# Performance work log

Measured on AMD Instinct MI355X. Metric: run time of the kernel, lower is better.

## Reference

```python
import jax, jax.numpy as jnp
import numpy as np

B, C, H, W = 1, 1, 1024, 1024
NP = 16                    # n_patches
S = NP * NP                # 256 tokens
D = 2048                   # hidden_d
NH = 16                    # heads
DH = D // NH               # 128
MLP = 4 * D
NB = 2                     # blocks
INPUT_D = C * (H // NP) * (W // NP)  # 4096
EPS = 1e-5


def positional_embeddings(s, d):
    # result[i,j] = sin(i/10000**(j/d)) if j even else cos(i/10000**((j-1)/d))
    i = jnp.arange(s, dtype=jnp.float32)[:, None]
    j = jnp.arange(d, dtype=jnp.float32)[None, :]
    even = (jnp.arange(d) % 2 == 0)[None, :]
    expo = jnp.where(even, j, j - 1.0) / d
    ang = i / (10000.0 ** expo)
    return jnp.where(even, jnp.sin(ang), jnp.cos(ang))


def layer_norm(x, g, b):
    m = x.mean(-1, keepdims=True)
    v = ((x - m) ** 2).mean(-1, keepdims=True)
    return (x - m) / jnp.sqrt(v + EPS) * g + b


def setup_inputs() -> dict:
    key = jax.random.key(0)
    ks = jax.random.split(key, 20)
    s = 0.02
    return {
        "images": jax.random.normal(ks[0], (B, C, H, W), jnp.float32),
        "memory": jax.random.normal(ks[1], (1, 8), jnp.float32),
        "wmap": jax.random.normal(ks[2], (INPUT_D, D), jnp.float32) * s,
        "bmap": jnp.zeros((D,), jnp.float32),
        "ln1_g": jnp.ones((NB, D), jnp.float32),
        "ln1_b": jnp.zeros((NB, D), jnp.float32),
        "qw": jax.random.normal(ks[3], (NB, NH, DH, DH), jnp.float32) * s,
        "qb": jnp.zeros((NB, NH, DH), jnp.float32),
        "kw": jax.random.normal(ks[4], (NB, NH, DH, DH), jnp.float32) * s,
        "kb": jnp.zeros((NB, NH, DH), jnp.float32),
        "vw": jax.random.normal(ks[5], (NB, NH, DH, DH), jnp.float32) * s,
        "vb": jnp.zeros((NB, NH, DH), jnp.float32),
        "ln2_g": jnp.ones((NB, D), jnp.float32),
        "ln2_b": jnp.zeros((NB, D), jnp.float32),
        "w1": jax.random.normal(ks[6], (NB, D, MLP), jnp.float32) * s,
        "b1": jnp.zeros((NB, MLP), jnp.float32),
        "w2": jax.random.normal(ks[7], (NB, MLP, D), jnp.float32) * s,
        "b2": jnp.zeros((NB, D), jnp.float32),
        "head_w": jax.random.normal(ks[8], (D, 1), jnp.float32) * s,
        "head_b": jnp.zeros((1,), jnp.float32),
    }


def reference(images, memory, wmap, bmap, ln1_g, ln1_b, qw, qb, kw, kb, vw, vb,
              ln2_g, ln2_b, w1, b1, w2, b2, head_w, head_b):
    # patchify: view(1, n_patches**2, num_h*num_v) -> (1, 256, 4096)
    patches = images.reshape(1, S, INPUT_D)
    tokens = patches @ wmap + bmap                      # (1, S, D)
    x = tokens + positional_embeddings(S, D)
    scale = DH ** 0.5
    for l in range(NB):
        h = layer_norm(x, ln1_g[l], ln1_b[l])
        h4 = h.reshape(B, S, NH, DH)
        q = jnp.einsum('bshd,hde->bshe', h4, qw[l]) + qb[l]
        k = jnp.einsum('bshd,hde->bshe', h4, kw[l]) + kb[l]
        v = jnp.einsum('bshd,hde->bshe', h4, vw[l]) + vb[l]
        att = jax.nn.softmax(jnp.einsum('bshe,bthe->bhst', q, k) / scale, axis=-1)
        attn_out = jnp.einsum('bhst,bthe->bshe', att, v).reshape(B, S, D)
        x = x + attn_out
        h2 = layer_norm(x, ln2_g[l], ln2_b[l])
        x = x + (jax.nn.gelu(h2 @ w1[l] + b1[l], approximate=False) @ w2[l] + b2[l])
    cls = x[:, 0]                                       # (1, D)
    out = jax.nn.sigmoid(cls @ head_w + head_b)         # (1, 1)
    return (out, memory)
```

## Files before the change

kernel.cpp:

```cpp
#include <hip/hip_runtime.h>
#include <math.h>

#define SQ   256
#define DD   2048
#define NHD  16
#define DHD  128
#define MLPD 8192
#define KIN  4096
#define INV_SQRT_DH 0.08838834764831845f

typedef __attribute__((ext_vector_type(8))) short bf16x8;
typedef __attribute__((ext_vector_type(4))) float f32x4;

__device__ __forceinline__ float gelu_f(float x) {
    return 0.5f * x * (1.0f + erff(x * 0.70710678118654752f));
}

__device__ __forceinline__ short f2bf(float f) {
    unsigned u = __float_as_uint(f);
    unsigned r = (u + 0x7fffu + ((u >> 16) & 1u)) >> 16;
    return (short)r;
}

__global__ __launch_bounds__(256) void gemm_splitk(const float* __restrict__ A,
                                                   const float* __restrict__ W,
                                                   float* __restrict__ C,
                                                   int N, int K, int KC) {
    __shared__ short As[64 * 64];
    __shared__ short Bs[64 * 64];
    const int tid = threadIdx.x;
    const int n0 = blockIdx.x * 64, m0 = blockIdx.y * 64;
    const int kstart = blockIdx.z * KC;
    const int wv = tid >> 6, ln = tid & 63;
    const int l15 = ln & 15, q = ln >> 4;

    f32x4 acc[4];
    #pragma unroll
    for (int j = 0; j < 4; j++) acc[j] = (f32x4){0.f, 0.f, 0.f, 0.f};

    const int am = tid >> 2, akb = (tid & 3) * 16, ac0 = (tid & 3) * 2;
    const int bn = tid & 63, bkb = (tid >> 6) * 16, bc0 = (tid >> 6) * 2;
    short* as0 = &As[am * 64 + ((ac0 ^ (am & 7)) * 8)];
    short* as1 = &As[am * 64 + (((ac0 + 1) ^ (am & 7)) * 8)];
    short* bs0 = &Bs[bn * 64 + ((bc0 ^ (bn & 7)) * 8)];
    short* bs1 = &Bs[bn * 64 + (((bc0 + 1) ^ (bn & 7)) * 8)];
    const int arow = 16 * wv + l15;
    const short* af0 = &As[arow * 64 + ((q ^ (arow & 7)) * 8)];
    const short* af1 = &As[arow * 64 + (((q + 4) ^ (arow & 7)) * 8)];

    for (int kc = kstart; kc < kstart + KC; kc += 64) {
        const float* ap = A + (size_t)(m0 + am) * K + kc + akb;
        float4 a0 = *(const float4*)ap;
        float4 a1 = *(const float4*)(ap + 4);
        float4 a2 = *(const float4*)(ap + 8);
        float4 a3 = *(const float4*)(ap + 12);
        const float* wp = W + (size_t)(kc + bkb) * N + n0 + bn;
        float wb[16];
        #pragma unroll
        for (int j = 0; j < 16; j++) wb[j] = wp[(size_t)j * N];

        __syncthreads();
        {
            short t[16] = {f2bf(a0.x), f2bf(a0.y), f2bf(a0.z), f2bf(a0.w),
                           f2bf(a1.x), f2bf(a1.y), f2bf(a1.z), f2bf(a1.w),
                           f2bf(a2.x), f2bf(a2.y), f2bf(a2.z), f2bf(a2.w),
                           f2bf(a3.x), f2bf(a3.y), f2bf(a3.z), f2bf(a3.w)};
            *(bf16x8*)as0 = *(bf16x8*)&t[0];
            *(bf16x8*)as1 = *(bf16x8*)&t[8];
            short u[16];
            #pragma unroll
            for (int j = 0; j < 16; j++) u[j] = f2bf(wb[j]);
            *(bf16x8*)bs0 = *(bf16x8*)&u[0];
            *(bf16x8*)bs1 = *(bf16x8*)&u[8];
        }
        __syncthreads();

        bf16x8 fa0 = *(const bf16x8*)af0;
        bf16x8 fa1 = *(const bf16x8*)af1;
        #pragma unroll
        for (int jt = 0; jt < 4; jt++) {
            const int brow = 16 * jt + l15;
            bf16x8 fb0 = *(const bf16x8*)&Bs[brow * 64 + ((q ^ (brow & 7)) * 8)];
            bf16x8 fb1 = *(const bf16x8*)&Bs[brow * 64 + (((q + 4) ^ (brow & 7)) * 8)];
            acc[jt] = __builtin_amdgcn_mfma_f32_16x16x32_bf16(fa0, fb0, acc[jt], 0, 0, 0);
            acc[jt] = __builtin_amdgcn_mfma_f32_16x16x32_bf16(fa1, fb1, acc[jt], 0, 0, 0);
        }
    }
    #pragma unroll
    for (int jt = 0; jt < 4; jt++) {
        const int n = n0 + 16 * jt + l15;
        #pragma unroll
        for (int i = 0; i < 4; i++) {
            const int m = m0 + 16 * wv + q * 4 + i;
            atomicAdd(&C[(size_t)m * N + n], acc[jt][i]);
        }
    }
}

__global__ __launch_bounds__(256) void epi_pos(float* __restrict__ x,
                                               const float* __restrict__ bmap) {
    const int idx = blockIdx.x * 256 + threadIdx.x;
    const int m = idx >> 11, n = idx & 2047;
    float val = x[idx] + bmap[n];
    float jf = (float)n;
    float expo = ((n & 1) ? (jf - 1.0f) : jf) * (1.0f / 2048.0f);
    float ang = (float)m * powf(10000.0f, -expo);
    x[idx] = val + ((n & 1) ? cosf(ang) : sinf(ang));
}

__global__ __launch_bounds__(256) void epi_gelu(float* __restrict__ y,
                                                const float* __restrict__ b1) {
    const int idx = blockIdx.x * 256 + threadIdx.x;
    y[idx] = gelu_f(y[idx] + b1[idx & 8191]);
}

__global__ __launch_bounds__(256) void epi_bias(float* __restrict__ x,
                                                const float* __restrict__ b2) {
    const int idx = blockIdx.x * 256 + threadIdx.x;
    x[idx] += b2[idx & 2047];
}

__global__ __launch_bounds__(256) void qkv_mfma(const float* __restrict__ h,
                                                const float* __restrict__ qw, const float* __restrict__ kw,
                                                const float* __restrict__ vw, const float* __restrict__ qb,
                                                const float* __restrict__ kb, const float* __restrict__ vb,
                                                float* __restrict__ q, float* __restrict__ k,
                                                float* __restrict__ v) {
    __shared__ short As[64 * 64];
    __shared__ short Bs[64 * 64];
    const int head = blockIdx.x, m0 = blockIdx.y * 64;
    const int type = blockIdx.z >> 1, n0 = (blockIdx.z & 1) * 64;
    const float* W; const float* B; float* O;
    if (type == 0)      { W = qw; B = qb; O = q; }
    else if (type == 1) { W = kw; B = kb; O = k; }
    else                { W = vw; B = vb; O = v; }
    W += (size_t)head * DHD * DHD;
    B += head * DHD;
    const int hoff = head * DHD;
    const int tid = threadIdx.x;
    const int wv = tid >> 6, ln = tid & 63;
    const int l15 = ln & 15, qq = ln >> 4;

    f32x4 acc[4];
    #pragma unroll
    for (int j = 0; j < 4; j++) acc[j] = (f32x4){0.f, 0.f, 0.f, 0.f};

    const int am = tid >> 2, akb = (tid & 3) * 16, ac0 = (tid & 3) * 2;
    const int bn = tid & 63, bkb = (tid >> 6) * 16, bc0 = (tid >> 6) * 2;
    short* as0 = &As[am * 64 + ((ac0 ^ (am & 7)) * 8)];
    short* as1 = &As[am * 64 + (((ac0 + 1) ^ (am & 7)) * 8)];
    short* bs0 = &Bs[bn * 64 + ((bc0 ^ (bn & 7)) * 8)];
    short* bs1 = &Bs[bn * 64 + (((bc0 + 1) ^ (bn & 7)) * 8)];
    const int arow = 16 * wv + l15;
    const short* af0 = &As[arow * 64 + ((qq ^ (arow & 7)) * 8)];
    const short* af1 = &As[arow * 64 + (((qq + 4) ^ (arow & 7)) * 8)];

    for (int kc = 0; kc < DHD; kc += 64) {
        const float* ap = h + (size_t)(m0 + am) * DD + hoff + kc + akb;
        float4 a0 = *(const float4*)ap;
        float4 a1 = *(const float4*)(ap + 4);
        float4 a2 = *(const float4*)(ap + 8);
        float4 a3 = *(const float4*)(ap + 12);
        const float* wp = W + (size_t)(kc + bkb) * DHD + n0 + bn;
        float wb[16];
        #pragma unroll
        for (int j = 0; j < 16; j++) wb[j] = wp[j * DHD];

        __syncthreads();
        {
            short t[16] = {f2bf(a0.x), f2bf(a0.y), f2bf(a0.z), f2bf(a0.w),
                           f2bf(a1.x), f2bf(a1.y), f2bf(a1.z), f2bf(a1.w),
                           f2bf(a2.x), f2bf(a2.y), f2bf(a2.z), f2bf(a2.w),
                           f2bf(a3.x), f2bf(a3.y), f2bf(a3.z), f2bf(a3.w)};
            *(bf16x8*)as0 = *(bf16x8*)&t[0];
            *(bf16x8*)as1 = *(bf16x8*)&t[8];
            short u[16];
            #pragma unroll
            for (int j = 0; j < 16; j++) u[j] = f2bf(wb[j]);
            *(bf16x8*)bs0 = *(bf16x8*)&u[0];
            *(bf16x8*)bs1 = *(bf16x8*)&u[8];
        }
        __syncthreads();

        bf16x8 fa0 = *(const bf16x8*)af0;
        bf16x8 fa1 = *(const bf16x8*)af1;
        #pragma unroll
        for (int jt = 0; jt < 4; jt++) {
            const int brow = 16 * jt + l15;
            bf16x8 fb0 = *(const bf16x8*)&Bs[brow * 64 + ((qq ^ (brow & 7)) * 8)];
            bf16x8 fb1 = *(const bf16x8*)&Bs[brow * 64 + (((qq + 4) ^ (brow & 7)) * 8)];
            acc[jt] = __builtin_amdgcn_mfma_f32_16x16x32_bf16(fa0, fb0, acc[jt], 0, 0, 0);
            acc[jt] = __builtin_amdgcn_mfma_f32_16x16x32_bf16(fa1, fb1, acc[jt], 0, 0, 0);
        }
    }
    #pragma unroll
    for (int jt = 0; jt < 4; jt++) {
        const int n = n0 + 16 * jt + l15;
        #pragma unroll
        for (int i = 0; i < 4; i++) {
            const int m = m0 + 16 * wv + qq * 4 + i;
            O[(size_t)m * DD + hoff + n] = acc[jt][i] + B[n];
        }
    }
}

__global__ __launch_bounds__(256) void attn_mfma(const float* __restrict__ q,
                                                 const float* __restrict__ k,
                                                 const float* __restrict__ v,
                                                 float* __restrict__ x) {
    __shared__ short P[64 * 272];
    __shared__ short ST[9216];
    const int head = blockIdx.y, r0 = blockIdx.x * 64;
    const int hoff = head * DHD;
    const int tid = threadIdx.x;
    const int wv = tid >> 6, ln = tid & 63;
    const int l15 = ln & 15, qd = ln >> 4;

    bf16x8 af[4];
    {
        const float* qp = q + (size_t)(r0 + 16 * wv + l15) * DD + hoff + qd * 8;
        #pragma unroll
        for (int s = 0; s < 4; s++) {
            float4 f0 = *(const float4*)(qp + s * 32);
            float4 f1 = *(const float4*)(qp + s * 32 + 4);
            short t[8] = {f2bf(f0.x), f2bf(f0.y), f2bf(f0.z), f2bf(f0.w),
                          f2bf(f1.x), f2bf(f1.y), f2bf(f1.z), f2bf(f1.w)};
            af[s] = *(bf16x8*)t;
        }
    }

    f32x4 sacc[16];
    #pragma unroll
    for (int i = 0; i < 16; i++) sacc[i] = (f32x4){0.f, 0.f, 0.f, 0.f};

    const int skey = tid >> 2, scol = (tid & 3) * 32;
    for (int kq = 0; kq < 4; kq++) {
        const float* kp = k + (size_t)(kq * 64 + skey) * DD + hoff + scol;
        float4 f[8];
        #pragma unroll
        for (int a = 0; a < 8; a++) f[a] = *(const float4*)(kp + a * 4);
        if (kq) __syncthreads();
        #pragma unroll
        for (int a = 0; a < 4; a++) {
            short t[8] = {f2bf(f[2*a].x), f2bf(f[2*a].y), f2bf(f[2*a].z), f2bf(f[2*a].w),
                          f2bf(f[2*a+1].x), f2bf(f[2*a+1].y), f2bf(f[2*a+1].z), f2bf(f[2*a+1].w)};
            *(bf16x8*)&ST[skey * 136 + scol + a * 8] = *(bf16x8*)t;
        }
        __syncthreads();
        #pragma unroll
        for (int nl = 0; nl < 4; nl++) {
            #pragma unroll
            for (int s = 0; s < 4; s++) {
                bf16x8 bfr = *(const bf16x8*)&ST[(nl * 16 + l15) * 136 + s * 32 + qd * 8];
                sacc[kq * 4 + nl] = __builtin_amdgcn_mfma_f32_16x16x32_bf16(af[s], bfr, sacc[kq * 4 + nl], 0, 0, 0);
            }
        }
    }

    float inv_s[4];
    #pragma unroll
    for (int i = 0; i < 4; i++) {
        float m = -1e30f;
        #pragma unroll
        for (int nt = 0; nt < 16; nt++) m = fmaxf(m, sacc[nt][i]);
        m = fmaxf(m, __shfl_xor(m, 1));
        m = fmaxf(m, __shfl_xor(m, 2));
        m = fmaxf(m, __shfl_xor(m, 4));
        m = fmaxf(m, __shfl_xor(m, 8));
        float sum = 0.f;
        #pragma unroll
        for (int nt = 0; nt < 16; nt++) {
            float e = __expf((sacc[nt][i] - m) * INV_SQRT_DH);
            sacc[nt][i] = e;
            sum += e;
        }
        sum += __shfl_xor(sum, 1);
        sum += __shfl_xor(sum, 2);
        sum += __shfl_xor(sum, 4);
        sum += __shfl_xor(sum, 8);
        inv_s[i] = 1.0f / sum;
    }
    #pragma unroll
    for (int nt = 0; nt < 16; nt++) {
        const int col = nt * 16 + l15;
        const int chunk = col >> 3, c7 = col & 7;
        #pragma unroll
        for (int i = 0; i < 4; i++) {
            const int row = 16 * wv + 4 * qd + i;
            P[row * 272 + ((chunk ^ (row & 7)) * 8) + c7] = f2bf(sacc[nt][i] * inv_s[i]);
        }
    }
    __syncthreads();

    f32x4 oacc[8];
    #pragma unroll
    for (int e = 0; e < 8; e++) oacc[e] = (f32x4){0.f, 0.f, 0.f, 0.f};

    const int ve = tid & 127, vks = (tid >> 7) * 32;
    for (int kq = 0; kq < 4; kq++) {
        float vv[32];
        #pragma unroll
        for (int j = 0; j < 32; j++)
            vv[j] = v[(size_t)(kq * 64 + vks + j) * DD + hoff + ve];
        if (kq) __syncthreads();
        #pragma unroll
        for (int c = 0; c < 4; c++) {
            short t[8];
            #pragma unroll
            for (int b = 0; b < 8; b++) t[b] = f2bf(vv[c * 8 + b]);
            const int ch = (vks >> 3) + c;
            *(bf16x8*)&ST[ve * 72 + ((ch ^ (ve & 7)) * 8)] = *(bf16x8*)t;
        }
        __syncthreads();
        #pragma unroll
        for (int s = 0; s < 2; s++) {
            const int row = 16 * wv + l15;
            const int pc = kq * 8 + s * 4 + qd;
            bf16x8 pa = *(const bf16x8*)&P[row * 272 + ((pc ^ (row & 7)) * 8)];
            #pragma unroll
            for (int et = 0; et < 8; et++) {
                const int er = et * 16 + l15;
                const int vc = s * 4 + qd;
                bf16x8 vb = *(const bf16x8*)&ST[er * 72 + ((vc ^ (er & 7)) * 8)];
                oacc[et] = __builtin_amdgcn_mfma_f32_16x16x32_bf16(pa, vb, oacc[et], 0, 0, 0);
            }
        }
    }
    #pragma unroll
    for (int et = 0; et < 8; et++) {
        const int e = et * 16 + l15;
        #pragma unroll
        for (int i = 0; i < 4; i++) {
            const int row = r0 + 16 * wv + 4 * qd + i;
            x[(size_t)row * DD + hoff + e] += oacc[et][i];
        }
    }
}

__global__ __launch_bounds__(256) void ln_kernel(const float* __restrict__ xin,
                                                 const float* __restrict__ g,
                                                 const float* __restrict__ b,
                                                 float* __restrict__ out,
                                                 float* __restrict__ zbuf, int zn) {
    __shared__ float red[8];
    const int tid = threadIdx.x;
    for (int i = tid; i < zn; i += 256) zbuf[i] = 0.0f;
    const int row = blockIdx.x;
    const float* xr = xin + row * DD;
    float vals[8];
    float s = 0.0f;
    #pragma unroll
    for (int i = 0; i < 8; i++) { vals[i] = xr[tid + i * 256]; s += vals[i]; }
    #pragma unroll
    for (int o = 32; o > 0; o >>= 1) s += __shfl_down(s, o);
    if ((tid & 63) == 0) red[tid >> 6] = s;
    __syncthreads();
    if (tid == 0) red[4] = (red[0] + red[1] + red[2] + red[3]) * (1.0f / 2048.0f);
    __syncthreads();
    const float mean = red[4];
    float vs = 0.0f;
    #pragma unroll
    for (int i = 0; i < 8; i++) { float d = vals[i] - mean; vs += d * d; }
    #pragma unroll
    for (int o = 32; o > 0; o >>= 1) vs += __shfl_down(vs, o);
    if ((tid & 63) == 0) red[tid >> 6] = vs;
    __syncthreads();
    if (tid == 0) red[5] = rsqrtf((red[0] + red[1] + red[2] + red[3]) * (1.0f / 2048.0f) + 1e-5f);
    __syncthreads();
    const float inv = red[5];
    #pragma unroll
    for (int i = 0; i < 8; i++) {
        int c = tid + i * 256;
        out[row * DD + c] = (vals[i] - mean) * inv * g[c] + b[c];
    }
}

__global__ __launch_bounds__(256) void attn0_kernel(const float* __restrict__ q,
                                                    const float* __restrict__ k,
                                                    const float* __restrict__ v,
                                                    float* __restrict__ x) {
    __shared__ float q0[128];
    __shared__ float p[256];
    __shared__ float red[8];
    const int h = blockIdx.x, tid = threadIdx.x, hoff = h * DHD;
    if (tid < 128) q0[tid] = q[hoff + tid];
    __syncthreads();
    const float* kr = k + tid * DD + hoff;
    float s = 0.0f;
    #pragma unroll 8
    for (int d = 0; d < 128; d++) s += q0[d] * kr[d];
    s *= INV_SQRT_DH;
    float m = s;
    #pragma unroll
    for (int o = 32; o > 0; o >>= 1) m = fmaxf(m, __shfl_down(m, o));
    if ((tid & 63) == 0) red[tid >> 6] = m;
    __syncthreads();
    if (tid == 0) red[4] = fmaxf(fmaxf(red[0], red[1]), fmaxf(red[2], red[3]));
    __syncthreads();
    const float mx = red[4];
    float e = __expf(s - mx);
    p[tid] = e;
    float t = e;
    #pragma unroll
    for (int o = 32; o > 0; o >>= 1) t += __shfl_down(t, o);
    if ((tid & 63) == 0) red[tid >> 6] = t;
    __syncthreads();
    if (tid == 0) red[5] = red[0] + red[1] + red[2] + red[3];
    __syncthreads();
    const float inv = 1.0f / red[5];
    if (tid < 128) {
        float acc = 0.0f;
        #pragma unroll 8
        for (int j = 0; j < 256; j++) acc += p[j] * v[j * DD + hoff + tid];
        x[hoff + tid] += acc * inv;
    }
}

__global__ __launch_bounds__(256) void gemv1_kernel(const float* __restrict__ h2,
                                                    const float* __restrict__ w1,
                                                    float* __restrict__ y) {
    const int n = blockIdx.x * 256 + threadIdx.x;
    const int k0 = blockIdx.y * 64;
    float s = 0.0f;
    #pragma unroll 8
    for (int k = 0; k < 64; k++) s += h2[k0 + k] * w1[(size_t)(k0 + k) * MLPD + n];
    atomicAdd(&y[n], s);
}

__global__ __launch_bounds__(256) void gelu_bias_kernel(float* __restrict__ y,
                                                        const float* __restrict__ b1) {
    const int n = blockIdx.x * 256 + threadIdx.x;
    y[n] = gelu_f(y[n] + b1[n]);
}

__global__ __launch_bounds__(256) void gemv2_kernel(const float* __restrict__ y1,
                                                    const float* __restrict__ w2,
                                                    float* __restrict__ x) {
    const int m = blockIdx.x * 256 + threadIdx.x;
    const int k0 = blockIdx.y * 256;
    float s = 0.0f;
    #pragma unroll 8
    for (int k = 0; k < 256; k++) s += y1[k0 + k] * w2[(size_t)(k0 + k) * DD + m];
    atomicAdd(&x[m], s);
}

__global__ __launch_bounds__(256) void head_kernel(const float* __restrict__ x,
                                                   const float* __restrict__ b2l,
                                                   const float* __restrict__ hw,
                                                   const float* __restrict__ hb,
                                                   const float* __restrict__ mem,
                                                   float* __restrict__ out) {
    __shared__ float red[8];
    const int tid = threadIdx.x;
    float s = 0.0f;
    for (int m = tid; m < 2048; m += 256) s += (x[m] + b2l[m]) * hw[m];
    #pragma unroll
    for (int o = 32; o > 0; o >>= 1) s += __shfl_down(s, o);
    if ((tid & 63) == 0) red[tid >> 6] = s;
    __syncthreads();
    if (tid == 0) {
        float t = red[0] + red[1] + red[2] + red[3];
        out[0] = 1.0f / (1.0f + __expf(-(t + hb[0])));
    }
    if (tid < 8) out[1 + tid] = mem[tid];
}

extern "C" void kernel_launch(void* const* d_in, const int* in_sizes, int n_in,
                              void* d_out, int out_size, void* d_ws, size_t ws_size,
                              hipStream_t stream) {
    const float* images = (const float*)d_in[0];
    const float* memory = (const float*)d_in[1];
    const float* wmap   = (const float*)d_in[2];
    const float* bmap   = (const float*)d_in[3];
    const float* ln1_g  = (const float*)d_in[4];
    const float* ln1_b  = (const float*)d_in[5];
    const float* qw     = (const float*)d_in[6];
    const float* qb     = (const float*)d_in[7];
    const float* kw     = (const float*)d_in[8];
    const float* kb     = (const float*)d_in[9];
    const float* vw     = (const float*)d_in[10];
    const float* vb     = (const float*)d_in[11];
    const float* ln2_g  = (const float*)d_in[12];
    const float* ln2_b  = (const float*)d_in[13];
    const float* w1     = (const float*)d_in[14];
    const float* b1     = (const float*)d_in[15];
    const float* w2     = (const float*)d_in[16];
    const float* b2     = (const float*)d_in[17];
    const float* head_w = (const float*)d_in[18];
    const float* head_b = (const float*)d_in[19];
    float* out = (float*)d_out;

    float* ws = (float*)d_ws;
    float* x     = ws;
    float* h     = x + SQ * DD;
    float* q     = h + SQ * DD;
    float* k     = q + SQ * DD;
    float* v     = k + SQ * DD;
    float* y1    = v + SQ * DD;
    float* y1row = y1 + SQ * MLPD;
    float* h2row = y1row + MLPD;

    hipMemsetAsync(x, 0, (size_t)SQ * DD * sizeof(float), stream);
    gemm_splitk<<<dim3(DD / 64, SQ / 64, 8), 256, 0, stream>>>(images, wmap, x, DD, KIN, 512);
    epi_pos<<<SQ * DD / 256, 256, 0, stream>>>(x, bmap);

    for (int l = 0; l < 2; l++) {
        const size_t wofs = (size_t)l * NHD * DHD * DHD;
        const size_t bofs = (size_t)l * NHD * DHD;
        ln_kernel<<<SQ, 256, 0, stream>>>(x, ln1_g + l * DD, ln1_b + l * DD, h, nullptr, 0);
        qkv_mfma<<<dim3(NHD, SQ / 64, 6), 256, 0, stream>>>(h, qw + wofs, kw + wofs, vw + wofs,
                                                            qb + bofs, kb + bofs, vb + bofs,
                                                            q, k, v);
        if (l == 0) {
            attn_mfma<<<dim3(SQ / 64, NHD), 256, 0, stream>>>(q, k, v, x);
            ln_kernel<<<SQ, 256, 0, stream>>>(x, ln2_g, ln2_b, h, nullptr, 0);
            hipMemsetAsync(y1, 0, (size_t)SQ * MLPD * sizeof(float), stream);
            gemm_splitk<<<dim3(MLPD / 64, SQ / 64, 2), 256, 0, stream>>>(h, w1, y1, MLPD, DD, 1024);
            epi_gelu<<<SQ * MLPD / 256, 256, 0, stream>>>(y1, b1);
            gemm_splitk<<<dim3(DD / 64, SQ / 64, 8), 256, 0, stream>>>(y1, w2, x, DD, MLPD, 1024);
            epi_bias<<<SQ * DD / 256, 256, 0, stream>>>(x, b2);
        } else {
            attn0_kernel<<<NHD, 256, 0, stream>>>(q, k, v, x);
            ln_kernel<<<1, 256, 0, stream>>>(x, ln2_g + DD, ln2_b + DD, h2row, y1row, MLPD);
            gemv1_kernel<<<dim3(MLPD / 256, 32), 256, 0, stream>>>(h2row, w1 + (size_t)DD * MLPD, y1row);
            gelu_bias_kernel<<<MLPD / 256, 256, 0, stream>>>(y1row, b1 + MLPD);
            gemv2_kernel<<<dim3(DD / 256, 32), 256, 0, stream>>>(y1row, w2 + (size_t)DD * MLPD, x);
            head_kernel<<<1, 256, 0, stream>>>(x, b2 + DD, head_w, head_b, memory, out);
        }
    }
}
```

Baseline: 508.3 us.

## Replace 64x64 split-K GEMM with double-buffered 128x128 tile GEMM

Swaps the 64x64-tile split-K GEMM for a 128x128-tile version with 512 threads, where each wave computes a 64x32 sub-tile. Shared-memory tiles are double-buffered and the next chunk's global loads are issued before the current chunk's MFMAs, so one sync per chunk replaces two. Larger tiles cut redundant global reads of A and W per FLOP, at the cost of a quarter as many blocks (fewer than CUs for the 2048-wide GEMMs) and more shared memory and registers per block.

```diff
diff --git a/kernel.cpp b/kernel.cpp
--- a/kernel.cpp
+++ b/kernel.cpp
@@ -22,77 +22,131 @@
     return (short)r;
 }
 
-__global__ __launch_bounds__(256) void gemm_splitk(const float* __restrict__ A,
-                                                   const float* __restrict__ W,
-                                                   float* __restrict__ C,
-                                                   int N, int K, int KC) {
-    __shared__ short As[64 * 64];
-    __shared__ short Bs[64 * 64];
+__global__ __launch_bounds__(512) void gemm128(const float* __restrict__ A,
+                                               const float* __restrict__ W,
+                                               float* __restrict__ C,
+                                               int N, int K, int KC) {
+    __shared__ short As[2][128 * 64];
+    __shared__ short Bs[2][128 * 64];
     const int tid = threadIdx.x;
-    const int n0 = blockIdx.x * 64, m0 = blockIdx.y * 64;
+    const int n0 = blockIdx.x * 128, m0 = blockIdx.y * 128;
     const int kstart = blockIdx.z * KC;
-    const int wv = tid >> 6, ln = tid & 63;
+    const int ln = tid & 63;
+    const int wv = tid >> 6;
     const int l15 = ln & 15, q = ln >> 4;
-
-    f32x4 acc[4];
-    #pragma unroll
-    for (int j = 0; j < 4; j++) acc[j] = (f32x4){0.f, 0.f, 0.f, 0.f};
-
-    const int am = tid >> 2, akb = (tid & 3) * 16, ac0 = (tid & 3) * 2;
-    const int bn = tid & 63, bkb = (tid >> 6) * 16, bc0 = (tid >> 6) * 2;
-    short* as0 = &As[am * 64 + ((ac0 ^ (am & 7)) * 8)];
-    short* as1 = &As[am * 64 + (((ac0 + 1) ^ (am & 7)) * 8)];
-    short* bs0 = &Bs[bn * 64 + ((bc0 ^ (bn & 7)) * 8)];
-    short* bs1 = &Bs[bn * 64 + (((bc0 + 1) ^ (bn & 7)) * 8)];
-    const int arow = 16 * wv + l15;
-    const short* af0 = &As[arow * 64 + ((q ^ (arow & 7)) * 8)];
-    const short* af1 = &As[arow * 64 + (((q + 4) ^ (arow & 7)) * 8)];
-
-    for (int kc = kstart; kc < kstart + KC; kc += 64) {
-        const float* ap = A + (size_t)(m0 + am) * K + kc + akb;
-        float4 a0 = *(const float4*)ap;
-        float4 a1 = *(const float4*)(ap + 4);
-        float4 a2 = *(const float4*)(ap + 8);
-        float4 a3 = *(const float4*)(ap + 12);
-        const float* wp = W + (size_t)(kc + bkb) * N + n0 + bn;
-        float wb[16];
-        #pragma unroll
-        for (int j = 0; j < 16; j++) wb[j] = wp[(size_t)j * N];
-
+    const int wm = wv >> 2, wn = wv & 3;
+
+    f32x4 acc[4][2];
+    #pragma unroll
+    for (int mt = 0; mt < 4; mt++)
+        #pragma unroll
+        for (int nt = 0; nt < 2; nt++) acc[mt][nt] = (f32x4){0.f, 0.f, 0.f, 0.f};
+
+    const int am = tid >> 2, ak0 = (tid & 3) * 16;
+    const int bn = tid & 127, bk0 = (tid >> 7) * 16;
+    const int aw0 = am * 64 + ((((ak0 >> 3) + 0) ^ (am & 7)) * 8);
+    const int aw1 = am * 64 + ((((ak0 >> 3) + 1) ^ (am & 7)) * 8);
+    const int bw0 = bn * 64 + ((((bk0 >> 3) + 0) ^ (bn & 7)) * 8);
+    const int bw1 = bn * 64 + ((((bk0 >> 3) + 1) ^ (bn & 7)) * 8);
+
+    const float* aptr = A + (size_t)(m0 + am) * K + kstart + ak0;
+    const float* wptr = W + (size_t)(kstart + bk0) * N + n0 + bn;
+
+    const int nch = KC >> 6;
+
+    float4 a[4];
+    float wb[16];
+    #pragma unroll
+    for (int j = 0; j < 4; j++) a[j] = *(const float4*)(aptr + 4 * j);
+    #pragma unroll
+    for (int j = 0; j < 16; j++) wb[j] = wptr[(size_t)j * N];
+    {
+        short t0[16];
+        #pragma unroll
+        for (int j = 0; j < 4; j++) {
+            t0[4 * j]     = f2bf(a[j].x);
+            t0[4 * j + 1] = f2bf(a[j].y);
+            t0[4 * j + 2] = f2bf(a[j].z);
+            t0[4 * j + 3] = f2bf(a[j].w);
+        }
+        *(bf16x8*)&As[0][aw0] = *(bf16x8*)&t0[0];
+        *(bf16x8*)&As[0][aw1] = *(bf16x8*)&t0[8];
+        short u0[16];
+        #pragma unroll
+        for (int j = 0; j < 16; j++) u0[j] = f2bf(wb[j]);
+        *(bf16x8*)&Bs[0][bw0] = *(bf16x8*)&u0[0];
+        *(bf16x8*)&Bs[0][bw1] = *(bf16x8*)&u0[8];
+    }
+    __syncthreads();
+
+    int cur = 0;
+    for (int t = 0; t < nch; t++) {
+        const bool pf = (t + 1 < nch);
+        if (pf) {
+            const float* ap = aptr + (t + 1) * 64;
+            #pragma unroll
+            for (int j = 0; j < 4; j++) a[j] = *(const float4*)(ap + 4 * j);
+            const float* wp = wptr + (size_t)(t + 1) * 64 * N;
+            #pragma unroll
+            for (int j = 0; j < 16; j++) wb[j] = wp[(size_t)j * N];
+        }
+
+        const short* Ab = As[cur];
+        const short* Bb = Bs[cur];
+        bf16x8 af[4][2], bf[2][2];
+        #pragma unroll
+        for (int mt = 0; mt < 4; mt++) {
+            const int ar = wm * 64 + mt * 16 + l15;
+            af[mt][0] = *(const bf16x8*)&Ab[ar * 64 + ((q ^ (ar & 7)) * 8)];
+            af[mt][1] = *(const bf16x8*)&Ab[ar * 64 + (((q + 4) ^ (ar & 7)) * 8)];
+        }
+        #pragma unroll
+        for (int nt = 0; nt < 2; nt++) {
+            const int br = wn * 32 + nt * 16 + l15;
+            bf[nt][0] = *(const bf16x8*)&Bb[br * 64 + ((q ^ (br & 7)) * 8)];
+            bf[nt][1] = *(const bf16x8*)&Bb[br * 64 + (((q + 4) ^ (br & 7)) * 8)];
+        }
+        #pragma unroll
+        for (int mt = 0; mt < 4; mt++)
+            #pragma unroll
+            for (int nt = 0; nt < 2; nt++) {
+                acc[mt][nt] = __builtin_amdgcn_mfma_f32_16x16x32_bf16(af[mt][0], bf[nt][0], acc[mt][nt], 0, 0, 0);
+                acc[mt][nt] = __builtin_amdgcn_mfma_f32_16x16x32_bf16(af[mt][1], bf[nt][1], acc[mt][nt], 0, 0, 0);
+            }
+
+        if (pf) {
+            short t1[16];
+            #pragma unroll
+            for (int j = 0; j < 4; j++) {
+                t1[4 * j]     = f2bf(a[j].x);
+                t1[4 * j + 1] = f2bf(a[j].y);
+                t1[4 * j + 2] = f2bf(a[j].z);
+                t1[4 * j + 3] = f2bf(a[j].w);
+            }
+            short* Aw = (short*)As[cur ^ 1];
+            short* Bw = (short*)Bs[cur ^ 1];
+            *(bf16x8*)&Aw[aw0] = *(bf16x8*)&t1[0];
+            *(bf16x8*)&Aw[aw1] = *(bf16x8*)&t1[8];
+            short u1[16];
+            #pragma unroll
+            for (int j = 0; j < 16; j++) u1[j] = f2bf(wb[j]);
+            *(bf16x8*)&Bw[bw0] = *(bf16x8*)&u1[0];
+            *(bf16x8*)&Bw[bw1] = *(bf16x8*)&u1[8];
+        }
         __syncthreads();
-        {
-            short t[16] = {f2bf(a0.x), f2bf(a0.y), f2bf(a0.z), f2bf(a0.w),
-                           f2bf(a1.x), f2bf(a1.y), f2bf(a1.z), f2bf(a1.w),
-                           f2bf(a2.x), f2bf(a2.y), f2bf(a2.z), f2bf(a2.w),
-                           f2bf(a3.x), f2bf(a3.y), f2bf(a3.z), f2bf(a3.w)};
-            *(bf16x8*)as0 = *(bf16x8*)&t[0];
-            *(bf16x8*)as1 = *(bf16x8*)&t[8];
-            short u[16];
-            #pragma unroll
-            for (int j = 0; j < 16; j++) u[j] = f2bf(wb[j]);
-            *(bf16x8*)bs0 = *(bf16x8*)&u[0];
-            *(bf16x8*)bs1 = *(bf16x8*)&u[8];
-        }
-        __syncthreads();
-
-        bf16x8 fa0 = *(const bf16x8*)af0;
-        bf16x8 fa1 = *(const bf16x8*)af1;
-        #pragma unroll
-        for (int jt = 0; jt < 4; jt++) {
-            const int brow = 16 * jt + l15;
-            bf16x8 fb0 = *(const bf16x8*)&Bs[brow * 64 + ((q ^ (brow & 7)) * 8)];
-            bf16x8 fb1 = *(const bf16x8*)&Bs[brow * 64 + (((q + 4) ^ (brow & 7)) * 8)];
-            acc[jt] = __builtin_amdgcn_mfma_f32_16x16x32_bf16(fa0, fb0, acc[jt], 0, 0, 0);
-            acc[jt] = __builtin_amdgcn_mfma_f32_16x16x32_bf16(fa1, fb1, acc[jt], 0, 0, 0);
-        }
-    }
-    #pragma unroll
-    for (int jt = 0; jt < 4; jt++) {
-        const int n = n0 + 16 * jt + l15;
-        #pragma unroll
-        for (int i = 0; i < 4; i++) {
-            const int m = m0 + 16 * wv + q * 4 + i;
-            atomicAdd(&C[(size_t)m * N + n], acc[jt][i]);
+        cur ^= 1;
+    }
+
+    #pragma unroll
+    for (int mt = 0; mt < 4; mt++) {
+        #pragma unroll
+        for (int nt = 0; nt < 2; nt++) {
+            const int col = n0 + wn * 32 + nt * 16 + l15;
+            #pragma unroll
+            for (int i = 0; i < 4; i++) {
+                const int row = m0 + wm * 64 + mt * 16 + q * 4 + i;
+                atomicAdd(&C[(size_t)row * N + col], acc[mt][nt][i]);
+            }
         }
     }
 }
@@ -501,7 +555,7 @@
     float* h2row = y1row + MLPD;
 
     hipMemsetAsync(x, 0, (size_t)SQ * DD * sizeof(float), stream);
-    gemm_splitk<<<dim3(DD / 64, SQ / 64, 8), 256, 0, stream>>>(images, wmap, x, DD, KIN, 512);
+    gemm128<<<dim3(DD / 128, SQ / 128, 8), 512, 0, stream>>>(images, wmap, x, DD, KIN, 512);
     epi_pos<<<SQ * DD / 256, 256, 0, stream>>>(x, bmap);
 
     for (int l = 0; l < 2; l++) {
@@ -515,9 +569,9 @@
             attn_mfma<<<dim3(SQ / 64, NHD), 256, 0, stream>>>(q, k, v, x);
             ln_kernel<<<SQ, 256, 0, stream>>>(x, ln2_g, ln2_b, h, nullptr, 0);
             hipMemsetAsync(y1, 0, (size_t)SQ * MLPD * sizeof(float), stream);
-            gemm_splitk<<<dim3(MLPD / 64, SQ / 64, 2), 256, 0, stream>>>(h, w1, y1, MLPD, DD, 1024);
+            gemm128<<<dim3(MLPD / 128, SQ / 128, 2), 512, 0, stream>>>(h, w1, y1, MLPD, DD, 1024);
             epi_gelu<<<SQ * MLPD / 256, 256, 0, stream>>>(y1, b1);
-            gemm_splitk<<<dim3(DD / 64, SQ / 64, 8), 256, 0, stream>>>(y1, w2, x, DD, MLPD, 1024);
+            gemm128<<<dim3(DD / 128, SQ / 128, 8), 512, 0, stream>>>(y1, w2, x, DD, MLPD, 1024);
             epi_bias<<<SQ * DD / 256, 256, 0, stream>>>(x, b2);
         } else {
             attn0_kernel<<<NHD, 256, 0, stream>>>(q, k, v, x);
```

Measured after the change: 497.7 us. -2.1%, faster.
